# Optimization experiments

Measured on AMD Instinct MI355X. Metric: run time of the kernel, lower is better.

The kernel has to match this reference:

```python
import jax, jax.numpy as jnp
import numpy as np

NUM_CLUSTERS = 50000
LN_EPS = 1e-5


def setup_inputs() -> dict:
    key = jax.random.key(0)
    ks = jax.random.split(key, 8)
    N, E, H = 1000000, 64, 64
    x = jax.random.normal(ks[0], (N, E), dtype=jnp.float32)
    cluster = jax.random.randint(ks[1], (N,), 0, NUM_CLUSTERS, dtype=jnp.int64)
    batch = jax.random.randint(ks[2], (N,), 0, 64, dtype=jnp.int64)
    W1 = jax.random.normal(ks[3], (E, H), dtype=jnp.float32) / np.sqrt(E)
    b1 = jnp.zeros((H,), dtype=jnp.float32)
    ln_g = jnp.ones((H,), dtype=jnp.float32)
    ln_b = jnp.zeros((H,), dtype=jnp.float32)
    W2 = jax.random.normal(ks[4], (H, E // 2), dtype=jnp.float32) / np.sqrt(H)
    b2 = jnp.zeros((E // 2,), dtype=jnp.float32)
    return {"x": x, "cluster": cluster, "batch": batch, "W1": W1, "b1": b1,
            "ln_g": ln_g, "ln_b": ln_b, "W2": W2, "b2": b2}


def _mlp(x, W1, b1, ln_g, ln_b, W2, b2):
    h = x @ W1 + b1                                   # [N, H]
    mu = jnp.mean(h, axis=-1, keepdims=True)
    var = jnp.mean(jnp.square(h - mu), axis=-1, keepdims=True)
    h = (h - mu) * jax.lax.rsqrt(var + LN_EPS) * ln_g + ln_b
    h = h * jax.nn.sigmoid(h)                         # SiLU
    return h @ W2 + b2                                # [N, E//2]


def reference(x, cluster, batch, W1, b1, ln_g, ln_b, W2, b2):
    out = _mlp(x, W1, b1, ln_g, ln_b, W2, b2)         # [N, E//2]
    cl = cluster.astype(jnp.int32)
    # max-pool per cluster (segment max), then gather back per node
    aggr = jax.ops.segment_max(out, cl, num_segments=NUM_CLUSTERS)  # [C, E//2]
    return jnp.concatenate([out, aggr[cl]], axis=-1)  # [N, E]
```

## Files before the change

kernel.cpp:

```cpp
#include <hip/hip_runtime.h>
#include <hip/hip_bf16.h>

#define NUM_CLUSTERS 50000

typedef __attribute__((ext_vector_type(8))) short bfx8;
typedef __attribute__((ext_vector_type(4))) float f32x4;

__device__ __forceinline__ unsigned fkey(float f) {
    unsigned b = __float_as_uint(f);
    return b ^ ((b & 0x80000000u) ? 0xFFFFFFFFu : 0x80000000u);
}
__device__ __forceinline__ float funkey(unsigned k) {
    unsigned b = (k & 0x80000000u) ? (k ^ 0x80000000u) : ~k;
    return __uint_as_float(b);
}
__device__ __forceinline__ unsigned short f2bf(float f) {
    unsigned u = __float_as_uint(f);
    return (unsigned short)((u + 0x7FFFu + ((u >> 16) & 1u)) >> 16);
}
__device__ __forceinline__ unsigned pk2bf(float a, float b) {
    __hip_bfloat162 h = __float22bfloat162_rn(make_float2(a, b));
    return *(unsigned*)&h;
}

__global__ __launch_bounds__(256) void prep_weights(
    const float* __restrict__ W1, const float* __restrict__ W2,
    unsigned short* __restrict__ w1f, unsigned short* __restrict__ w2f)
{
    int tid = blockIdx.x * 256 + threadIdx.x;
    if (tid < 512) {
        int frag = tid >> 6, lane = tid & 63;
        int ct = frag >> 1, kb = frag & 1;
        int col = ct * 16 + (lane & 15);
        int k0 = kb * 32 + (lane >> 4) * 8;
        #pragma unroll
        for (int i = 0; i < 8; ++i)
            w1f[(frag * 64 + lane) * 8 + i] = f2bf(W1[(k0 + i) * 64 + col]);
    } else if (tid < 768) {
        int frag = (tid - 512) >> 6, lane = tid & 63;
        int ct = frag >> 1, kb = frag & 1;
        int col = ct * 16 + (lane & 15);
        int k0 = kb * 32 + (lane >> 4) * 8;
        #pragma unroll
        for (int i = 0; i < 8; ++i)
            w2f[(frag * 64 + lane) * 8 + i] = f2bf(W2[(k0 + i) * 32 + col]);
    }
}

__global__ __launch_bounds__(256, 5) void mlp_segmax_kernel(
    const float* __restrict__ x, const int* __restrict__ cluster,
    const unsigned short* __restrict__ w1f, const float* __restrict__ b1,
    const float* __restrict__ ln_g, const float* __restrict__ ln_b,
    const unsigned short* __restrict__ w2f, const float* __restrict__ b2,
    float* __restrict__ out, unsigned* __restrict__ aggr, int N)
{
    __shared__ char smem[256 * 128];
    const int t = threadIdx.x;
    const int lane = t & 63;
    const int w = t >> 6;
    const int l15 = lane & 15;
    const int q = lane >> 4;
    const long long wbase = (long long)blockIdx.x * 256 + w * 64;
    if (wbase >= N) return;
    char* wmem = smem + w * 8192;

    #pragma unroll 4
    for (int p = 0; p < 16; ++p) {
        int le = (p * 64 + lane) * 4;
        f32x4 v = __builtin_nontemporal_load((const f32x4*)(x + wbase * 64 + le));
        int row = le >> 6;
        int k = le & 63;
        int g = k >> 3;
        int half = (k >> 2) & 1;
        int phys = row * 128 + ((g ^ (row & 7)) << 4) + (half << 3);
        *(uint2*)(wmem + phys) = make_uint2(pk2bf(v[0], v[1]), pk2bf(v[2], v[3]));
    }

    bfx8 W1F[4][2], W2F[2][2];
    #pragma unroll
    for (int ct = 0; ct < 4; ++ct)
        #pragma unroll
        for (int kb = 0; kb < 2; ++kb)
            W1F[ct][kb] = *(const bfx8*)(w1f + ((ct * 2 + kb) * 64 + lane) * 8);
    #pragma unroll
    for (int ct = 0; ct < 2; ++ct)
        #pragma unroll
        for (int kb = 0; kb < 2; ++kb)
            W2F[ct][kb] = *(const bfx8*)(w2f + ((ct * 2 + kb) * 64 + lane) * 8);

    float g4[4], bb4[4], b1c[4];
    #pragma unroll
    for (int tt = 0; tt < 4; ++tt) {
        g4[tt]  = ln_g[16 * tt + l15];
        bb4[tt] = ln_b[16 * tt + l15];
        b1c[tt] = b1[16 * tt + l15];
    }
    float b2c[2] = { b2[l15], b2[16 + l15] };

    #pragma unroll 1
    for (int g = 0; g < 4; ++g) {
        const int base = g * 16;
        const int arow = base + l15;
        const int arsw = arow & 7;

        int clr[4];
        #pragma unroll
        for (int r = 0; r < 4; ++r)
            clr[r] = cluster[wbase + base + q * 4 + r];
        unsigned olds[8];
        #pragma unroll
        for (int c2 = 0; c2 < 2; ++c2)
            #pragma unroll
            for (int r = 0; r < 4; ++r)
                olds[c2 * 4 + r] = aggr[(long long)clr[r] * 32 + c2 * 16 + l15];

        bfx8 af[2];
        #pragma unroll
        for (int kb = 0; kb < 2; ++kb)
            af[kb] = *(const bfx8*)(wmem + arow * 128 + (((kb * 4 + q) ^ arsw) << 4));

        f32x4 acc[4];
        #pragma unroll
        for (int tt = 0; tt < 4; ++tt) {
            float b = b1c[tt];
            acc[tt] = (f32x4){b, b, b, b};
        }
        #pragma unroll
        for (int kb = 0; kb < 2; ++kb)
            #pragma unroll
            for (int tt = 0; tt < 4; ++tt)
                acc[tt] = __builtin_amdgcn_mfma_f32_16x16x32_bf16(af[kb], W1F[tt][kb], acc[tt], 0, 0, 0);

        float s[4];
        #pragma unroll
        for (int r = 0; r < 4; ++r)
            s[r] = acc[0][r] + acc[1][r] + acc[2][r] + acc[3][r];
        #pragma unroll
        for (int m = 1; m < 16; m <<= 1)
            #pragma unroll
            for (int r = 0; r < 4; ++r) s[r] += __shfl_xor(s[r], m, 16);
        float mu[4];
        #pragma unroll
        for (int r = 0; r < 4; ++r) mu[r] = s[r] * (1.f / 64.f);
        float vv[4] = {0.f, 0.f, 0.f, 0.f};
        #pragma unroll
        for (int tt = 0; tt < 4; ++tt)
            #pragma unroll
            for (int r = 0; r < 4; ++r) {
                float d = acc[tt][r] - mu[r];
                vv[r] = fmaf(d, d, vv[r]);
            }
        #pragma unroll
        for (int m = 1; m < 16; m <<= 1)
            #pragma unroll
            for (int r = 0; r < 4; ++r) vv[r] += __shfl_xor(vv[r], m, 16);
        float rs[4];
        #pragma unroll
        for (int r = 0; r < 4; ++r) rs[r] = rsqrtf(vv[r] * (1.f / 64.f) + 1e-5f);

        #pragma unroll
        for (int tt = 0; tt < 4; ++tt)
            #pragma unroll
            for (int r = 0; r < 4; ++r) {
                float val = (acc[tt][r] - mu[r]) * rs[r] * g4[tt] + bb4[tt];
                val = val / (1.f + __expf(-val));
                int node = base + q * 4 + r;
                int col = 16 * tt + l15;
                int phys = node * 128 + ((((col >> 3)) ^ (node & 7)) << 4) + ((col & 7) * 2);
                *(unsigned short*)(wmem + phys) = f2bf(val);
            }

        bfx8 hf[2];
        #pragma unroll
        for (int kb = 0; kb < 2; ++kb)
            hf[kb] = *(const bfx8*)(wmem + arow * 128 + (((kb * 4 + q) ^ arsw) << 4));
        f32x4 oacc[2];
        #pragma unroll
        for (int c2 = 0; c2 < 2; ++c2) {
            float b = b2c[c2];
            oacc[c2] = (f32x4){b, b, b, b};
        }
        #pragma unroll
        for (int kb = 0; kb < 2; ++kb)
            #pragma unroll
            for (int c2 = 0; c2 < 2; ++c2)
                oacc[c2] = __builtin_amdgcn_mfma_f32_16x16x32_bf16(hf[kb], W2F[c2][kb], oacc[c2], 0, 0, 0);

        #pragma unroll
        for (int c2 = 0; c2 < 2; ++c2)
            #pragma unroll
            for (int r = 0; r < 4; ++r) {
                int node = base + q * 4 + r;
                int byte = (c2 * 16 + l15) * 4;
                int phys = node * 128 + (((byte >> 4) ^ (node & 7)) << 4) + (byte & 15);
                *(float*)(wmem + phys) = oacc[c2][r];
            }

        #pragma unroll
        for (int c2 = 0; c2 < 2; ++c2)
            #pragma unroll
            for (int r = 0; r < 4; ++r) {
                unsigned key = fkey(oacc[c2][r]);
                if (key > olds[c2 * 4 + r])
                    atomicMax(aggr + (long long)clr[r] * 32 + c2 * 16 + l15, key);
            }
    }

    #pragma unroll 2
    for (int p = 0; p < 8; ++p) {
        int le = (p * 64 + lane) * 4;
        int row = le >> 5;
        int c = le & 31;
        f32x4 v4 = *(const f32x4*)(wmem + row * 128 + (((c >> 2) ^ (row & 7)) << 4));
        __builtin_nontemporal_store(v4, (f32x4*)(out + (wbase + row) * 64 + c));
    }
}

__global__ __launch_bounds__(256) void gather_kernel(
    const int* __restrict__ cluster, const unsigned* __restrict__ aggr,
    float* __restrict__ out, int N)
{
    long long idx = (long long)blockIdx.x * 256 + threadIdx.x;
    if (idx >= (long long)N * 8) return;
    int n = (int)(idx >> 3);
    int k4 = (int)(idx & 7) * 4;
    int c = cluster[n];
    uint4 a = *(const uint4*)(aggr + (size_t)c * 32 + k4);
    f32x4 o = {funkey(a.x), funkey(a.y), funkey(a.z), funkey(a.w)};
    __builtin_nontemporal_store(o, (f32x4*)(out + (size_t)n * 64 + 32 + k4));
}

extern "C" void kernel_launch(void* const* d_in, const int* in_sizes, int n_in,
                              void* d_out, int out_size, void* d_ws, size_t ws_size,
                              hipStream_t stream) {
    const float* x     = (const float*)d_in[0];
    const int* cluster = (const int*)d_in[1];
    const float* W1    = (const float*)d_in[3];
    const float* b1    = (const float*)d_in[4];
    const float* ln_g  = (const float*)d_in[5];
    const float* ln_b  = (const float*)d_in[6];
    const float* W2    = (const float*)d_in[7];
    const float* b2    = (const float*)d_in[8];
    float* out = (float*)d_out;

    unsigned* aggr = (unsigned*)d_ws;
    unsigned short* w1f = (unsigned short*)((char*)d_ws + (size_t)NUM_CLUSTERS * 32 * 4);
    unsigned short* w2f = w1f + 8 * 64 * 8;

    int N = in_sizes[0] / 64;

    hipMemsetAsync(aggr, 0, (size_t)NUM_CLUSTERS * 32 * sizeof(unsigned), stream);
    prep_weights<<<3, 256, 0, stream>>>(W1, W2, w1f, w2f);

    int blocks1 = (N + 255) / 256;
    mlp_segmax_kernel<<<blocks1, 256, 0, stream>>>(
        x, cluster, w1f, b1, ln_g, ln_b, w2f, b2, out, aggr, N);

    long long total2 = (long long)N * 8;
    int blocks2 = (int)((total2 + 255) / 256);
    gather_kernel<<<blocks2, 256, 0, stream>>>(cluster, aggr, out, N);
}
```

Baseline: 281.1 us.

## Replace atomic segment-max with counting-sort and per-cluster reduction

Drops the per-element atomicMax into the cluster aggregate buffer from the MLP kernel. Instead it builds a counting sort of node indices by cluster (histogram, single-block prefix scan, placement) and then runs a per-cluster kernel that re-reads the MLP outputs through the sorted index list to compute the max. This removes atomic contention and the ordered-key encoding, but adds several launches, a serial single-block scan, and a scattered re-read of the 128 MB output. An empty cluster would now yield -inf instead of the zero-key value.

```diff
diff --git a/kernel.cpp b/kernel.cpp
--- a/kernel.cpp
+++ b/kernel.cpp
@@ -1,19 +1,11 @@
 #include <hip/hip_runtime.h>
 #include <hip/hip_bf16.h>
 
-#define NUM_CLUSTERS 50000
+#define NC 50000
 
 typedef __attribute__((ext_vector_type(8))) short bfx8;
 typedef __attribute__((ext_vector_type(4))) float f32x4;
 
-__device__ __forceinline__ unsigned fkey(float f) {
-    unsigned b = __float_as_uint(f);
-    return b ^ ((b & 0x80000000u) ? 0xFFFFFFFFu : 0x80000000u);
-}
-__device__ __forceinline__ float funkey(unsigned k) {
-    unsigned b = (k & 0x80000000u) ? (k ^ 0x80000000u) : ~k;
-    return __uint_as_float(b);
-}
 __device__ __forceinline__ unsigned short f2bf(float f) {
     unsigned u = __float_as_uint(f);
     return (unsigned short)((u + 0x7FFFu + ((u >> 16) & 1u)) >> 16);
@@ -47,12 +39,55 @@
     }
 }
 
-__global__ __launch_bounds__(256, 5) void mlp_segmax_kernel(
-    const float* __restrict__ x, const int* __restrict__ cluster,
+__global__ __launch_bounds__(256) void hist_kernel(
+    const int* __restrict__ cluster, unsigned* __restrict__ cnt, int N)
+{
+    int i = blockIdx.x * 256 + threadIdx.x;
+    if (i < N) atomicAdd(&cnt[cluster[i]], 1u);
+}
+
+__global__ __launch_bounds__(1024) void prefix_kernel(
+    const unsigned* __restrict__ cnt, unsigned* __restrict__ offs,
+    unsigned* __restrict__ cursor)
+{
+    __shared__ unsigned ls[1024];
+    const int t = threadIdx.x;
+    const int S = 49;
+    unsigned base = (unsigned)t * S;
+    unsigned sum = 0;
+    for (int k = 0; k < S; ++k) { unsigned i = base + k; if (i < NC) sum += cnt[i]; }
+    ls[t] = sum;
+    __syncthreads();
+    for (int off = 1; off < 1024; off <<= 1) {
+        unsigned v = (t >= off) ? ls[t - off] : 0u;
+        __syncthreads();
+        ls[t] += v;
+        __syncthreads();
+    }
+    unsigned run = (t == 0) ? 0u : ls[t - 1];
+    for (int k = 0; k < S; ++k) {
+        unsigned i = base + k;
+        if (i < NC) { offs[i] = run; cursor[i] = run; run += cnt[i]; }
+    }
+}
+
+__global__ __launch_bounds__(256) void place_kernel(
+    const int* __restrict__ cluster, unsigned* __restrict__ cursor,
+    unsigned* __restrict__ sorted, int N)
+{
+    int i = blockIdx.x * 256 + threadIdx.x;
+    if (i < N) {
+        unsigned p = atomicAdd(&cursor[cluster[i]], 1u);
+        sorted[p] = (unsigned)i;
+    }
+}
+
+__global__ __launch_bounds__(256, 5) void mlp_kernel(
+    const float* __restrict__ x,
     const unsigned short* __restrict__ w1f, const float* __restrict__ b1,
     const float* __restrict__ ln_g, const float* __restrict__ ln_b,
     const unsigned short* __restrict__ w2f, const float* __restrict__ b2,
-    float* __restrict__ out, unsigned* __restrict__ aggr, int N)
+    float* __restrict__ out, int N)
 {
     __shared__ char smem[256 * 128];
     const int t = threadIdx.x;
@@ -103,17 +138,6 @@
         const int arow = base + l15;
         const int arsw = arow & 7;
 
-        int clr[4];
-        #pragma unroll
-        for (int r = 0; r < 4; ++r)
-            clr[r] = cluster[wbase + base + q * 4 + r];
-        unsigned olds[8];
-        #pragma unroll
-        for (int c2 = 0; c2 < 2; ++c2)
-            #pragma unroll
-            for (int r = 0; r < 4; ++r)
-                olds[c2 * 4 + r] = aggr[(long long)clr[r] * 32 + c2 * 16 + l15];
-
         bfx8 af[2];
         #pragma unroll
         for (int kb = 0; kb < 2; ++kb)
@@ -195,15 +219,6 @@
                 int phys = node * 128 + (((byte >> 4) ^ (node & 7)) << 4) + (byte & 15);
                 *(float*)(wmem + phys) = oacc[c2][r];
             }
-
-        #pragma unroll
-        for (int c2 = 0; c2 < 2; ++c2)
-            #pragma unroll
-            for (int r = 0; r < 4; ++r) {
-                unsigned key = fkey(oacc[c2][r]);
-                if (key > olds[c2 * 4 + r])
-                    atomicMax(aggr + (long long)clr[r] * 32 + c2 * 16 + l15, key);
-            }
     }
 
     #pragma unroll 2
@@ -216,8 +231,29 @@
     }
 }
 
+__global__ __launch_bounds__(256) void aggr_kernel(
+    const unsigned* __restrict__ offs, const unsigned* __restrict__ cnt,
+    const unsigned* __restrict__ sorted, const float* __restrict__ out,
+    float* __restrict__ aggrf)
+{
+    int c = blockIdx.x * 4 + (threadIdx.x >> 6);
+    if (c >= NC) return;
+    const int lane = threadIdx.x & 63;
+    const int half = lane >> 5;
+    const int slot = lane & 31;
+    unsigned n0 = offs[c];
+    unsigned k = cnt[c];
+    float m = -__builtin_huge_valf();
+    for (unsigned j = half; j < k; j += 2) {
+        unsigned idx = sorted[n0 + j];
+        m = fmaxf(m, out[(size_t)idx * 64 + slot]);
+    }
+    m = fmaxf(m, __shfl_xor(m, 32));
+    if (lane < 32) aggrf[(size_t)c * 32 + slot] = m;
+}
+
 __global__ __launch_bounds__(256) void gather_kernel(
-    const int* __restrict__ cluster, const unsigned* __restrict__ aggr,
+    const int* __restrict__ cluster, const float* __restrict__ aggrf,
     float* __restrict__ out, int N)
 {
     long long idx = (long long)blockIdx.x * 256 + threadIdx.x;
@@ -225,9 +261,8 @@
     int n = (int)(idx >> 3);
     int k4 = (int)(idx & 7) * 4;
     int c = cluster[n];
-    uint4 a = *(const uint4*)(aggr + (size_t)c * 32 + k4);
-    f32x4 o = {funkey(a.x), funkey(a.y), funkey(a.z), funkey(a.w)};
-    __builtin_nontemporal_store(o, (f32x4*)(out + (size_t)n * 64 + 32 + k4));
+    f32x4 a = *(const f32x4*)(aggrf + (size_t)c * 32 + k4);
+    __builtin_nontemporal_store(a, (f32x4*)(out + (size_t)n * 64 + 32 + k4));
 }
 
 extern "C" void kernel_launch(void* const* d_in, const int* in_sizes, int n_in,
@@ -243,20 +278,31 @@
     const float* b2    = (const float*)d_in[8];
     float* out = (float*)d_out;
 
-    unsigned* aggr = (unsigned*)d_ws;
-    unsigned short* w1f = (unsigned short*)((char*)d_ws + (size_t)NUM_CLUSTERS * 32 * 4);
-    unsigned short* w2f = w1f + 8 * 64 * 8;
+    char* ws = (char*)d_ws;
+    unsigned short* w1f = (unsigned short*)ws;
+    unsigned short* w2f = (unsigned short*)(ws + 8192);
+    unsigned* cnt    = (unsigned*)(ws + 16384);
+    unsigned* offs   = (unsigned*)(ws + 216384);
+    unsigned* cursor = (unsigned*)(ws + 416384);
+    unsigned* sorted = (unsigned*)(ws + 616384);
+    float*    aggrf  = (float*)(ws + 4616384);
 
     int N = in_sizes[0] / 64;
 
-    hipMemsetAsync(aggr, 0, (size_t)NUM_CLUSTERS * 32 * sizeof(unsigned), stream);
+    hipMemsetAsync(cnt, 0, (size_t)NC * sizeof(unsigned), stream);
     prep_weights<<<3, 256, 0, stream>>>(W1, W2, w1f, w2f);
 
-    int blocks1 = (N + 255) / 256;
-    mlp_segmax_kernel<<<blocks1, 256, 0, stream>>>(
-        x, cluster, w1f, b1, ln_g, ln_b, w2f, b2, out, aggr, N);
+    int nblocks = (N + 255) / 256;
+    hist_kernel<<<nblocks, 256, 0, stream>>>(cluster, cnt, N);
+    prefix_kernel<<<1, 1024, 0, stream>>>(cnt, offs, cursor);
+    place_kernel<<<nblocks, 256, 0, stream>>>(cluster, cursor, sorted, N);
+
+    mlp_kernel<<<nblocks, 256, 0, stream>>>(
+        x, w1f, b1, ln_g, ln_b, w2f, b2, out, N);
+
+    aggr_kernel<<<(NC + 3) / 4, 256, 0, stream>>>(offs, cnt, sorted, out, aggrf);
 
     long long total2 = (long long)N * 8;
     int blocks2 = (int)((total2 + 255) / 256);
-    gather_kernel<<<blocks2, 256, 0, stream>>>(cluster, aggr, out, N);
-}
+    gather_kernel<<<blocks2, 256, 0, stream>>>(cluster, aggrf, out, N);
+}
```

Result: slower. 549.3 us (+95.4%).
